# Performance work log

Measured on AMD Instinct MI355X. Metric: run time of the kernel, lower is better.

The kernel has to match this reference:

```python
import jax, jax.numpy as jnp
import numpy as np

STRIDE = 16      # image -> feature stride (224 -> 14)
POOL = 7         # ROI pool output grid
FG_HI = 0.85
FG_LO = 0.5


def setup_inputs() -> dict:
    key = jax.random.key(0)
    ks = jax.random.split(key, 8)
    B, N, M, K = 4, 128, 16, 80
    Cf, Tf, Cs, Ts, H, W = 256, 32, 2048, 8, 14, 14
    fast = jax.random.normal(ks[0], (B, Cf, Tf, H, W), jnp.float32)
    slow = jax.random.normal(ks[1], (B, Cs, Ts, H, W), jnp.float32)
    # valid gt boxes inside 224x224
    xy = jax.random.uniform(ks[2], (B, M, 2)) * 160.0
    wh = 32.0 + jax.random.uniform(ks[3], (B, M, 2)) * 48.0
    gt = jnp.concatenate([xy, xy + wh], axis=-1)
    # proposals: first M coincide with gt (guarantees IoU>=0.85 foreground), rest random
    pxy = jax.random.uniform(ks[4], (B, N - M, 2)) * 160.0
    pwh = 16.0 + jax.random.uniform(ks[5], (B, N - M, 2)) * 64.0
    props = jnp.concatenate([gt, jnp.concatenate([pxy, pxy + pwh], axis=-1)], axis=1)
    gt_classes = (jax.random.uniform(ks[6], (B, M, K)) < 0.1).astype(jnp.float32)
    C = Cf + Cs
    W_cls = jax.random.normal(ks[7], (C, K), jnp.float32) * 0.02
    b_cls = jnp.zeros((K,), jnp.float32)
    return dict(fast_feature=fast, slow_feature=slow, proposal_bboxes=props,
                gt_bboxes_batch=gt, gt_classes_batch=gt_classes,
                W_cls=W_cls, b_cls=b_cls)


def _iou(a, b):
    # a: [B,N,4], b: [B,M,4] (x1,y1,x2,y2) -> [B,N,M]
    tl = jnp.maximum(a[:, :, None, :2], b[:, None, :, :2])
    br = jnp.minimum(a[:, :, None, 2:], b[:, None, :, 2:])
    inter = jnp.prod(jnp.clip(br - tl, 0.0), axis=-1)
    area_a = jnp.prod(a[:, :, 2:] - a[:, :, :2], axis=-1)[:, :, None]
    area_b = jnp.prod(b[:, :, 2:] - b[:, :, :2], axis=-1)[:, None, :]
    return inter / (area_a + area_b - inter)


def _roi_pool(feat, boxes):
    # feat: [B,C,H,W]; boxes: [B,N,4] in image coords -> [B,N,P,P,C]
    B, C, H, W = feat.shape
    fb = boxes / STRIDE
    x1, y1, x2, y2 = fb[..., 0], fb[..., 1], fb[..., 2], fb[..., 3]
    grid = (jnp.arange(POOL, dtype=feat.dtype) + 0.5) / POOL          # [P]
    cy = y1[..., None] + grid * (y2 - y1)[..., None]                  # [B,N,P]
    cx = x1[..., None] + grid * (x2 - x1)[..., None]                  # [B,N,P]
    iy = jnp.clip(jnp.floor(cy), 0, H - 1).astype(jnp.int32)
    ix = jnp.clip(jnp.floor(cx), 0, W - 1).astype(jnp.int32)
    ft = jnp.transpose(feat, (0, 2, 3, 1))                            # [B,H,W,C]
    bidx = jnp.arange(B)[:, None, None, None]
    return ft[bidx, iy[:, :, :, None], ix[:, :, None, :]]             # [B,N,P,P,C]


def reference(fast_feature, slow_feature, proposal_bboxes, gt_bboxes_batch,
              gt_classes_batch, W_cls, b_cls):
    # temporal average pooling (AvgPool3d over full T) + channel concat, fast first
    fast = fast_feature.mean(axis=2)
    slow = slow_feature.mean(axis=2)
    feature = jnp.concatenate([fast, slow], axis=1)                   # [B,C,H,W]

    # IoU-based foreground assignment
    ious = _iou(proposal_bboxes, gt_bboxes_batch)                     # [B,N,M]
    max_ious = ious.max(axis=2)                                       # [B,N]
    assign = ious.argmax(axis=2)                                      # [B,N]
    fg_hi = max_ious >= FG_HI
    fg = jnp.where(fg_hi.any(), fg_hi, max_ious >= FG_LO)             # global fallback
    labels = jnp.take_along_axis(gt_classes_batch, assign[:, :, None], axis=1)  # [B,N,K]

    # ROI pooling (dense over all proposals; non-fg are masked out of the loss)
    pool = _roi_pool(feature, proposal_bboxes)                        # [B,N,P,P,C]
    hid = pool.mean(axis=(2, 3))                                      # [B,N,C]
    logits = jnp.einsum('bnc,ck->bnk', hid, W_cls) + b_cls            # [B,N,K]

    # multilabel soft margin loss per proposal (mean over classes)
    per = -(labels * jax.nn.log_sigmoid(logits)
            + (1.0 - labels) * jax.nn.log_sigmoid(-logits)).mean(axis=-1)  # [B,N]
    fgf = fg.astype(per.dtype)
    cnt = fgf.sum(axis=1)
    cross_entropies = jnp.where(cnt > 0, (per * fgf).sum(axis=1) / jnp.maximum(cnt, 1.0), 0.0)
    return cross_entropies  # [B]
```

## Files before the change

kernel.cpp:

```cpp
#include <hip/hip_runtime.h>
#include <math.h>

#define BB 4
#define NN 128
#define MM 16
#define KK 80
#define CF 256
#define CSL 2048
#define CT 2304
#define TFAST 32
#define TSLOW 8
#define HH 14
#define WW 14
#define HWQ 196
#define NQ4 49

#define FEAT_OFF   0
#define FEAT_SIZE  (BB*CT*HWQ)
#define G_OFF      (FEAT_OFF + FEAT_SIZE)
#define G_SIZE     (BB*HWQ*KK)
#define FGF_OFF    (G_OFF + G_SIZE)
#define ASSIGN_OFF (FGF_OFF + BB*NN)
#define NUM_OFF    (ASSIGN_OFF + BB*NN)
#define CNT_OFF    (NUM_OFF + BB)
#define CTR_OFF    (CNT_OFF + BB)
#define P_OFF      (CTR_OFF + 8)

#define NSPLIT 32
#define CCH    (CT/NSPLIT)
#define P_SIZE (NSPLIT*G_SIZE)

__global__ __launch_bounds__(256) void k1_tmean(const float* __restrict__ fast,
                                                const float* __restrict__ slow,
                                                float* __restrict__ ws) {
    int idx = blockIdx.x * blockDim.x + threadIdx.x;
    if (idx < G_SIZE) ws[G_OFF + idx] = 0.f;
    const int total = BB * CT * NQ4;
    if (idx >= total) return;
    int q  = idx % NQ4;
    int bc = idx / NQ4;
    int c  = bc % CT;
    int b  = bc / CT;
    float4 acc = make_float4(0.f, 0.f, 0.f, 0.f);
    if (c < CF) {
        const float4* p = (const float4*)(fast + (size_t)(b*CF + c) * TFAST * HWQ) + q;
        #pragma unroll 8
        for (int t = 0; t < TFAST; ++t) {
            float4 v = p[t * (HWQ/4)];
            acc.x += v.x; acc.y += v.y; acc.z += v.z; acc.w += v.w;
        }
        const float s = 1.f / TFAST;
        acc.x *= s; acc.y *= s; acc.z *= s; acc.w *= s;
    } else {
        const float4* p = (const float4*)(slow + (size_t)(b*CSL + (c-CF)) * TSLOW * HWQ) + q;
        #pragma unroll
        for (int t = 0; t < TSLOW; ++t) {
            float4 v = p[t * (HWQ/4)];
            acc.x += v.x; acc.y += v.y; acc.z += v.z; acc.w += v.w;
        }
        const float s = 1.f / TSLOW;
        acc.x *= s; acc.y *= s; acc.z *= s; acc.w *= s;
    }
    ((float4*)(ws + FEAT_OFF))[bc * NQ4 + q] = acc;
}

__global__ __launch_bounds__(256) void k2_gemm(const float* __restrict__ Wc,
                                               float* __restrict__ ws,
                                               int use_partials) {
    __shared__ float sfeat[CCH*HWQ];
    __shared__ float sW[CCH*KK];
    int bid = blockIdx.x;
    int b  = bid >> 6;
    int r  = bid & 63;
    int kh = r >> 5;
    int cs = r & 31;
    int c0 = cs * CCH;
    int tid = threadIdx.x;

    const float4* fsrc = (const float4*)(ws + FEAT_OFF + (size_t)(b*CT + c0) * HWQ);
    float4* fdst = (float4*)sfeat;
    #pragma unroll
    for (int i = 0; i < 14; ++i) {
        int x = tid + i*256;
        if (x < CCH*HWQ/4) fdst[x] = fsrc[x];
    }
    const float4* wsrc = (const float4*)(Wc + c0*KK);
    float4* wdst = (float4*)sW;
    #pragma unroll
    for (int i = 0; i < 6; ++i) {
        int x = tid + i*256;
        if (x < CCH*KK/4) wdst[x] = wsrc[x];
    }
    __syncthreads();

    int kq = tid & 7;
    int cg = tid >> 3;
    float acc[7][5];
    #pragma unroll
    for (int j = 0; j < 7; ++j)
        #pragma unroll
        for (int i = 0; i < 5; ++i) acc[j][i] = 0.f;

    const float* fr = sfeat + cg;
    const float* wr = sW + kh*40 + kq*5;
    #pragma unroll 2
    for (int c = 0; c < CCH; ++c) {
        float w0 = wr[c*KK+0], w1 = wr[c*KK+1], w2 = wr[c*KK+2],
              w3 = wr[c*KK+3], w4 = wr[c*KK+4];
        #pragma unroll
        for (int j = 0; j < 7; ++j) {
            float fv = fr[c*HWQ + 32*j];
            acc[j][0] += fv*w0; acc[j][1] += fv*w1; acc[j][2] += fv*w2;
            acc[j][3] += fv*w3; acc[j][4] += fv*w4;
        }
    }

    int k0 = kh*40 + kq*5;
    if (use_partials) {
        float* P = ws + P_OFF + (size_t)cs*G_SIZE + (size_t)b*HWQ*KK;
        #pragma unroll
        for (int j = 0; j < 7; ++j) {
            int cell = cg + 32*j;
            if (cell < HWQ) {
                #pragma unroll
                for (int i = 0; i < 5; ++i) P[cell*KK + k0 + i] = acc[j][i];
            }
        }
    } else {
        float* g = ws + G_OFF + (size_t)b*HWQ*KK;
        #pragma unroll
        for (int j = 0; j < 7; ++j) {
            int cell = cg + 32*j;
            if (cell < HWQ) {
                #pragma unroll
                for (int i = 0; i < 5; ++i) atomicAdd(&g[cell*KK + k0 + i], acc[j][i]);
            }
        }
    }
}

#define RED_BLOCKS ((G_SIZE + 511) / 512)
__global__ __launch_bounds__(512) void k2b_assign(const float* __restrict__ props,
                                                  const float* __restrict__ gtb,
                                                  float* __restrict__ ws,
                                                  int use_partials) {
    int blk = blockIdx.x;
    int t = threadIdx.x;
    if (blk < RED_BLOCKS) {
        if (!use_partials) return;
        int idx = blk * 512 + t;
        if (idx < G_SIZE) {
            const float* P = ws + P_OFF;
            float s = 0.f;
            #pragma unroll
            for (int cs = 0; cs < NSPLIT; ++cs) s += P[(size_t)cs*G_SIZE + idx];
            ws[G_OFF + idx] = s;
        }
        return;
    }
    __shared__ float sgt[BB*MM*4];
    __shared__ float sfg[BB*NN];
    __shared__ int sany;
    if (t < BB*MM*4) sgt[t] = gtb[t];
    if (t == 0) sany = 0;
    __syncthreads();
    int b = t >> 7;
    float x1 = props[t*4+0], y1 = props[t*4+1], x2 = props[t*4+2], y2 = props[t*4+3];
    float aa = (x2 - x1) * (y2 - y1);
    float best = -1.f; int arg = 0;
    for (int m = 0; m < MM; ++m) {
        const float* g = &sgt[(b*MM + m)*4];
        float tlx = fmaxf(x1, g[0]), tly = fmaxf(y1, g[1]);
        float brx = fminf(x2, g[2]), bry = fminf(y2, g[3]);
        float inter = fmaxf(brx - tlx, 0.f) * fmaxf(bry - tly, 0.f);
        float ab = (g[2] - g[0]) * (g[3] - g[1]);
        float iou = inter / (aa + ab - inter);
        if (iou > best) { best = iou; arg = m; }
    }
    if (best >= 0.85f) atomicOr(&sany, 1);
    __syncthreads();
    float fg = sany ? (best >= 0.85f ? 1.f : 0.f) : (best >= 0.5f ? 1.f : 0.f);
    sfg[t] = fg;
    ws[FGF_OFF + t] = fg;
    ((int*)ws)[ASSIGN_OFF + t] = arg;
    __syncthreads();
    if (t < BB) {
        float s = 0.f;
        for (int i = 0; i < NN; ++i) s += sfg[t*NN + i];
        ws[CNT_OFF + t] = s;
        ws[NUM_OFF + t] = 0.f;
    }
    if (t == 0) ((int*)ws)[CTR_OFF] = 0;
}

__device__ __forceinline__ float logsig(float x) {
    return fminf(x, 0.f) - log1pf(expf(-fabsf(x)));
}

__global__ __launch_bounds__(128) void k3b_loss(const float* __restrict__ props,
                                                const float* __restrict__ gtc,
                                                const float* __restrict__ bcls,
                                                float* __restrict__ ws,
                                                float* __restrict__ out) {
    int p = blockIdx.x;
    int b = p >> 7;
    int t = threadIdx.x;
    __shared__ int cells[49];
    __shared__ float red[128];
    if (ws[FGF_OFF + p] != 0.f) {
        if (t < 49) {
            int gy = t / 7, gx = t % 7;
            float x1 = props[p*4+0] * (1.f/16.f);
            float y1 = props[p*4+1] * (1.f/16.f);
            float x2 = props[p*4+2] * (1.f/16.f);
            float y2 = props[p*4+3] * (1.f/16.f);
            float gry = ((float)gy + 0.5f) / 7.f;
            float grx = ((float)gx + 0.5f) / 7.f;
            float cy = y1 + gry * (y2 - y1);
            float cx = x1 + grx * (x2 - x1);
            int iy = (int)floorf(cy); iy = min(max(iy, 0), HH-1);
            int ix = (int)floorf(cx); ix = min(max(ix, 0), WW-1);
            cells[t] = iy * WW + ix;
        }
        __syncthreads();
        float lk = 0.f;
        if (t < KK) {
            float acc = 0.f;
            const float* Gb = ws + G_OFF + b * HWQ * KK + t;
            #pragma unroll 7
            for (int g = 0; g < 49; ++g) acc += Gb[cells[g] * KK];
            float logit = acc * (1.f/49.f) + bcls[t];
            int a = ((const int*)ws)[ASSIGN_OFF + p];
            float y = gtc[(b*MM + a)*KK + t];
            lk = -(y * logsig(logit) + (1.f - y) * logsig(-logit));
        }
        red[t] = lk;
        __syncthreads();
        for (int s = 64; s > 0; s >>= 1) {
            if (t < s) red[t] += red[t + s];
            __syncthreads();
        }
        if (t == 0) atomicAdd(&ws[NUM_OFF + b], red[0] * (1.f/KK));
    }
    if (t == 0) {
        __threadfence();
        int old = atomicAdd(&((int*)ws)[CTR_OFF], 1);
        if (old == BB*NN - 1) {
            __threadfence();
            #pragma unroll
            for (int bb = 0; bb < BB; ++bb) {
                float num = atomicAdd(&ws[NUM_OFF + bb], 0.f);
                float c = ws[CNT_OFF + bb];
                out[bb] = (c > 0.f) ? num / c : 0.f;
            }
        }
    }
}

extern "C" void kernel_launch(void* const* d_in, const int* in_sizes, int n_in,
                              void* d_out, int out_size, void* d_ws, size_t ws_size,
                              hipStream_t stream) {
    const float* fast  = (const float*)d_in[0];
    const float* slow  = (const float*)d_in[1];
    const float* props = (const float*)d_in[2];
    const float* gtb   = (const float*)d_in[3];
    const float* gtc   = (const float*)d_in[4];
    const float* Wc    = (const float*)d_in[5];
    const float* bcls  = (const float*)d_in[6];
    float* ws  = (float*)d_ws;
    float* out = (float*)d_out;

    const size_t need = (size_t)(P_OFF + P_SIZE) * sizeof(float);
    const int use_partials = (ws_size >= need) ? 1 : 0;

    const int k1_threads = BB * CT * NQ4;
    k1_tmean<<<(k1_threads + 255)/256, 256, 0, stream>>>(fast, slow, ws);
    k2_gemm<<<BB * 2 * NSPLIT, 256, 0, stream>>>(Wc, ws, use_partials);
    k2b_assign<<<RED_BLOCKS + 1, 512, 0, stream>>>(props, gtb, ws, use_partials);
    k3b_loss<<<BB*NN, 128, 0, stream>>>(props, gtc, bcls, ws, out);
}
```

Before: 143.4 us.

## Fuse temporal mean into channel-split GEMM and transpose partial layout

Merges the temporal-mean kernel into the GEMM kernel, so each block averages its own channel slice straight into shared memory instead of writing and re-reading a full feature tensor in global memory. Channels are split unevenly so fast-path blocks (16 channels, 32 frames) and slow-path blocks (42-43 channels, 8 frames) carry comparable load. Each block now covers all 80 classes, with partials stored k-major for coalesced writes and transposed back during the reduction. Grid size drops to 256 blocks with larger register tiles (7x10 accumulators), which lowers occupancy and puts the mean's memory latency and the GEMM in the same block.

```diff
diff --git a/kernel.cpp b/kernel.cpp
--- a/kernel.cpp
+++ b/kernel.cpp
@@ -15,9 +15,7 @@
 #define HWQ 196
 #define NQ4 49
 
-#define FEAT_OFF   0
-#define FEAT_SIZE  (BB*CT*HWQ)
-#define G_OFF      (FEAT_OFF + FEAT_SIZE)
+#define G_OFF      0
 #define G_SIZE     (BB*HWQ*KK)
 #define FGF_OFF    (G_OFF + G_SIZE)
 #define ASSIGN_OFF (FGF_OFF + BB*NN)
@@ -26,117 +24,102 @@
 #define CTR_OFF    (CNT_OFF + BB)
 #define P_OFF      (CTR_OFF + 8)
 
-#define NSPLIT 32
-#define CCH    (CT/NSPLIT)
+#define NSPLIT 64
+#define MAXCH  43
 #define P_SIZE (NSPLIT*G_SIZE)
 
-__global__ __launch_bounds__(256) void k1_tmean(const float* __restrict__ fast,
-                                                const float* __restrict__ slow,
-                                                float* __restrict__ ws) {
-    int idx = blockIdx.x * blockDim.x + threadIdx.x;
-    if (idx < G_SIZE) ws[G_OFF + idx] = 0.f;
-    const int total = BB * CT * NQ4;
-    if (idx >= total) return;
-    int q  = idx % NQ4;
-    int bc = idx / NQ4;
-    int c  = bc % CT;
-    int b  = bc / CT;
-    float4 acc = make_float4(0.f, 0.f, 0.f, 0.f);
-    if (c < CF) {
-        const float4* p = (const float4*)(fast + (size_t)(b*CF + c) * TFAST * HWQ) + q;
+__global__ __launch_bounds__(256) void k12_fused(const float* __restrict__ fastp,
+                                                 const float* __restrict__ slowp,
+                                                 const float* __restrict__ Wc,
+                                                 float* __restrict__ ws,
+                                                 int use_partials) {
+    __shared__ float sfeat[MAXCH*HWQ + 64];
+    __shared__ float sW[MAXCH*KK];
+    int bid = blockIdx.x;
+    int b = bid >> 6;
+    int r = bid & 63;
+    int gc0, nch, T, isfast;
+    if (r < 16) { isfast = 1; gc0 = r * 16; nch = 16; T = TFAST; }
+    else {
+        int s = r - 16;
+        int c0s = (s < 32) ? (43 * s) : (1376 + 42 * (s - 32));
+        nch = (s < 32) ? 43 : 42;
+        gc0 = CF + c0s; T = TSLOW; isfast = 0;
+    }
+    int tid = threadIdx.x;
+
+    const float4* base = isfast
+        ? ((const float4*)fastp + (size_t)(b * CF + gc0) * TFAST * NQ4)
+        : ((const float4*)slowp + (size_t)(b * CSL + (gc0 - CF)) * TSLOW * NQ4);
+    const float scale = 1.f / (float)T;
+    int ntasks = nch * NQ4;
+    for (int x = tid; x < ntasks; x += 256) {
+        int cl = x / NQ4;
+        int q  = x - cl * NQ4;
+        const float4* p = base + (size_t)cl * T * NQ4 + q;
+        float4 a = make_float4(0.f, 0.f, 0.f, 0.f);
         #pragma unroll 8
-        for (int t = 0; t < TFAST; ++t) {
-            float4 v = p[t * (HWQ/4)];
-            acc.x += v.x; acc.y += v.y; acc.z += v.z; acc.w += v.w;
-        }
-        const float s = 1.f / TFAST;
-        acc.x *= s; acc.y *= s; acc.z *= s; acc.w *= s;
-    } else {
-        const float4* p = (const float4*)(slow + (size_t)(b*CSL + (c-CF)) * TSLOW * HWQ) + q;
-        #pragma unroll
-        for (int t = 0; t < TSLOW; ++t) {
-            float4 v = p[t * (HWQ/4)];
-            acc.x += v.x; acc.y += v.y; acc.z += v.z; acc.w += v.w;
-        }
-        const float s = 1.f / TSLOW;
-        acc.x *= s; acc.y *= s; acc.z *= s; acc.w *= s;
-    }
-    ((float4*)(ws + FEAT_OFF))[bc * NQ4 + q] = acc;
-}
-
-__global__ __launch_bounds__(256) void k2_gemm(const float* __restrict__ Wc,
-                                               float* __restrict__ ws,
-                                               int use_partials) {
-    __shared__ float sfeat[CCH*HWQ];
-    __shared__ float sW[CCH*KK];
-    int bid = blockIdx.x;
-    int b  = bid >> 6;
-    int r  = bid & 63;
-    int kh = r >> 5;
-    int cs = r & 31;
-    int c0 = cs * CCH;
-    int tid = threadIdx.x;
-
-    const float4* fsrc = (const float4*)(ws + FEAT_OFF + (size_t)(b*CT + c0) * HWQ);
-    float4* fdst = (float4*)sfeat;
-    #pragma unroll
-    for (int i = 0; i < 14; ++i) {
-        int x = tid + i*256;
-        if (x < CCH*HWQ/4) fdst[x] = fsrc[x];
-    }
-    const float4* wsrc = (const float4*)(Wc + c0*KK);
-    float4* wdst = (float4*)sW;
-    #pragma unroll
-    for (int i = 0; i < 6; ++i) {
-        int x = tid + i*256;
-        if (x < CCH*KK/4) wdst[x] = wsrc[x];
-    }
-    __syncthreads();
-
-    int kq = tid & 7;
-    int cg = tid >> 3;
-    float acc[7][5];
+        for (int t = 0; t < T; ++t) {
+            float4 v = p[t * NQ4];
+            a.x += v.x; a.y += v.y; a.z += v.z; a.w += v.w;
+        }
+        a.x *= scale; a.y *= scale; a.z *= scale; a.w *= scale;
+        ((float4*)sfeat)[cl * NQ4 + q] = a;
+    }
+    const float4* wsrc = (const float4*)Wc + (size_t)gc0 * (KK / 4);
+    int wtasks = nch * (KK / 4);
+    for (int x = tid; x < wtasks; x += 256) ((float4*)sW)[x] = wsrc[x];
+    __syncthreads();
+
+    int cg = tid & 31;
+    int kq = tid >> 5;
+    float acc[7][10];
     #pragma unroll
     for (int j = 0; j < 7; ++j)
         #pragma unroll
-        for (int i = 0; i < 5; ++i) acc[j][i] = 0.f;
+        for (int i = 0; i < 10; ++i) acc[j][i] = 0.f;
 
     const float* fr = sfeat + cg;
-    const float* wr = sW + kh*40 + kq*5;
-    #pragma unroll 2
-    for (int c = 0; c < CCH; ++c) {
-        float w0 = wr[c*KK+0], w1 = wr[c*KK+1], w2 = wr[c*KK+2],
-              w3 = wr[c*KK+3], w4 = wr[c*KK+4];
+    const float* wr = sW + kq * 10;
+    for (int c = 0; c < nch; ++c) {
+        float w[10];
+        #pragma unroll
+        for (int i = 0; i < 10; ++i) w[i] = wr[c * KK + i];
         #pragma unroll
         for (int j = 0; j < 7; ++j) {
-            float fv = fr[c*HWQ + 32*j];
-            acc[j][0] += fv*w0; acc[j][1] += fv*w1; acc[j][2] += fv*w2;
-            acc[j][3] += fv*w3; acc[j][4] += fv*w4;
-        }
-    }
-
-    int k0 = kh*40 + kq*5;
+            float fv = fr[c * HWQ + 32 * j];
+            #pragma unroll
+            for (int i = 0; i < 10; ++i) acc[j][i] += fv * w[i];
+        }
+    }
+
+    int k0 = kq * 10;
     if (use_partials) {
-        float* P = ws + P_OFF + (size_t)cs*G_SIZE + (size_t)b*HWQ*KK;
+        float* P = ws + P_OFF + (size_t)r * G_SIZE + (size_t)b * (KK * HWQ);
         #pragma unroll
         for (int j = 0; j < 7; ++j) {
-            int cell = cg + 32*j;
+            int cell = cg + 32 * j;
             if (cell < HWQ) {
                 #pragma unroll
-                for (int i = 0; i < 5; ++i) P[cell*KK + k0 + i] = acc[j][i];
+                for (int i = 0; i < 10; ++i) P[(k0 + i) * HWQ + cell] = acc[j][i];
             }
         }
     } else {
-        float* g = ws + G_OFF + (size_t)b*HWQ*KK;
+        float* g = ws + G_OFF + (size_t)b * HWQ * KK;
         #pragma unroll
         for (int j = 0; j < 7; ++j) {
-            int cell = cg + 32*j;
+            int cell = cg + 32 * j;
             if (cell < HWQ) {
                 #pragma unroll
-                for (int i = 0; i < 5; ++i) atomicAdd(&g[cell*KK + k0 + i], acc[j][i]);
+                for (int i = 0; i < 10; ++i) atomicAdd(&g[cell * KK + k0 + i], acc[j][i]);
             }
         }
     }
+}
+
+__global__ __launch_bounds__(256) void kz_zero(float* __restrict__ ws) {
+    int idx = blockIdx.x * 256 + threadIdx.x;
+    if (idx < G_SIZE) ws[G_OFF + idx] = 0.f;
 }
 
 #define RED_BLOCKS ((G_SIZE + 511) / 512)
@@ -148,13 +131,17 @@
     int t = threadIdx.x;
     if (blk < RED_BLOCKS) {
         if (!use_partials) return;
-        int idx = blk * 512 + t;
-        if (idx < G_SIZE) {
+        int ridx = blk * 512 + t;
+        if (ridx < G_SIZE) {
             const float* P = ws + P_OFF;
             float s = 0.f;
-            #pragma unroll
-            for (int cs = 0; cs < NSPLIT; ++cs) s += P[(size_t)cs*G_SIZE + idx];
-            ws[G_OFF + idx] = s;
+            #pragma unroll 16
+            for (int cs = 0; cs < NSPLIT; ++cs) s += P[(size_t)cs * G_SIZE + ridx];
+            int b    = ridx / (KK * HWQ);
+            int rem  = ridx - b * (KK * HWQ);
+            int k    = rem / HWQ;
+            int cell = rem - k * HWQ;
+            ws[G_OFF + (size_t)b * HWQ * KK + cell * KK + k] = s;
         }
         return;
     }
@@ -260,8 +247,8 @@
 extern "C" void kernel_launch(void* const* d_in, const int* in_sizes, int n_in,
                               void* d_out, int out_size, void* d_ws, size_t ws_size,
                               hipStream_t stream) {
-    const float* fast  = (const float*)d_in[0];
-    const float* slow  = (const float*)d_in[1];
+    const float* fastp = (const float*)d_in[0];
+    const float* slowp = (const float*)d_in[1];
     const float* props = (const float*)d_in[2];
     const float* gtb   = (const float*)d_in[3];
     const float* gtc   = (const float*)d_in[4];
@@ -273,9 +260,9 @@
     const size_t need = (size_t)(P_OFF + P_SIZE) * sizeof(float);
     const int use_partials = (ws_size >= need) ? 1 : 0;
 
-    const int k1_threads = BB * CT * NQ4;
-    k1_tmean<<<(k1_threads + 255)/256, 256, 0, stream>>>(fast, slow, ws);
-    k2_gemm<<<BB * 2 * NSPLIT, 256, 0, stream>>>(Wc, ws, use_partials);
+    if (!use_partials)
+        kz_zero<<<(G_SIZE + 255)/256, 256, 0, stream>>>(ws);
+    k12_fused<<<BB * NSPLIT, 256, 0, stream>>>(fastp, slowp, Wc, ws, use_partials);
     k2b_assign<<<RED_BLOCKS + 1, 512, 0, stream>>>(props, gtb, ws, use_partials);
     k3b_loss<<<BB*NN, 128, 0, stream>>>(props, gtc, bcls, ws, out);
 }
```

New measurement: 134.0 us. 1.07x faster.
